# Performance work log

Hardware: AMD Instinct MI355X
Metric: run time of the kernel (lower is better)

## Reference

```python
import jax, jax.numpy as jnp
import numpy as np

B, N, C = 4, 2048, 1024
H = 16
D = C // H  # head dim = 64

def setup_inputs() -> dict:
    key = jax.random.key(0)
    k1, k2, k3 = jax.random.split(key, 3)
    x = jax.random.normal(k1, (B, N, C), dtype=jnp.float32)
    w_attn = jax.random.normal(k2, (C, 3 * C), dtype=jnp.float32) * (C ** -0.5)
    w_proj = jax.random.normal(k3, (C, C), dtype=jnp.float32) * (C ** -0.5)
    return {"x": x, "w_attn": w_attn, "w_proj": w_proj}

def reference(x, w_attn, w_proj):
    # fused QKV projection (bias=False)
    qkv = jnp.einsum('bnc,cf->bnf', x, w_attn)            # [B,N,3C]
    q, k, v = jnp.split(qkv, 3, axis=-1)                  # each [B,N,C]
    # [B,H,N,D]
    q = q.reshape(B, N, H, D).transpose(0, 2, 1, 3)
    k = k.reshape(B, N, H, D).transpose(0, 2, 1, 3)
    v = v.reshape(B, N, H, D).transpose(0, 2, 1, 3)
    # scaled dot-product attention, non-causal, no mask, dropout_p=0
    scale = 1.0 / jnp.sqrt(jnp.asarray(D, dtype=q.dtype))
    scores = jnp.einsum('bhqd,bhkd->bhqk', q, k) * scale  # [B,H,N,N]
    attn = jax.nn.softmax(scores, axis=-1)
    y = jnp.einsum('bhqk,bhkd->bhqd', attn, v)            # [B,H,N,D]
    y = y.transpose(0, 2, 1, 3).reshape(B, N, C)
    # output projection (bias=False); resid dropout is identity at p=0
    return jnp.einsum('bnc,co->bno', y, w_proj)
```

## Files before the change

kernel.cpp:

```cpp
#include <hip/hip_runtime.h>
#include <hip/hip_bf16.h>

typedef __hip_bfloat16 bf16;
typedef short short8 __attribute__((ext_vector_type(8)));
typedef float f32x4 __attribute__((ext_vector_type(4)));
typedef float f32x16 __attribute__((ext_vector_type(16)));

#define GLOBAL_AS __attribute__((address_space(1)))
#define LDS_AS __attribute__((address_space(3)))

__device__ inline unsigned short f2bf(float x) {
    union { float f; unsigned u; } v; v.f = x;
    unsigned r = v.u + 0x7fffu + ((v.u >> 16) & 1u);
    return (unsigned short)(r >> 16);
}

__device__ inline unsigned pkbf(float a, float b) {
    float2 f; f.x = a; f.y = b;
    union { __hip_bfloat162 h; unsigned u; } c;
    c.h = __float22bfloat162_rn(f);
    return c.u;
}

__device__ inline float fast_exp2(float x) {
#if __has_builtin(__builtin_amdgcn_exp2f)
    return __builtin_amdgcn_exp2f(x);
#else
    return exp2f(x);
#endif
}

__device__ inline void async16(const void* g, void* l) {
    __builtin_amdgcn_global_load_lds((const GLOBAL_AS void*)g, (LDS_AS void*)l, 16, 0, 0);
}


__global__ __launch_bounds__(256) void cvt_f32_bf16(const float* __restrict__ in,
                                                    unsigned short* __restrict__ out, int n4) {
    int i = blockIdx.x * 256 + threadIdx.x;
    if (i < n4) {
        float4 v = ((const float4*)in)[i];
        ushort4 o;
        o.x = f2bf(v.x); o.y = f2bf(v.y); o.z = f2bf(v.z); o.w = f2bf(v.w);
        ((ushort4*)out)[i] = o;
    }
}

__global__ __launch_bounds__(256) void transpose_bf16(const float* __restrict__ in,
                                                      unsigned short* __restrict__ out,
                                                      int R, int Cc) {
    __shared__ float s[32][33];
    int tx = threadIdx.x & 31, ty = threadIdx.x >> 5;
    int c0 = blockIdx.x * 32, r0 = blockIdx.y * 32;
#pragma unroll
    for (int i = 0; i < 4; i++)
        s[ty + i * 8][tx] = in[(size_t)(r0 + ty + i * 8) * Cc + c0 + tx];
    __syncthreads();
#pragma unroll
    for (int i = 0; i < 4; i++)
        out[(size_t)(c0 + ty + i * 8) * R + r0 + tx] = f2bf(s[tx][ty + i * 8]);
}


template <int MODE>
__global__ __launch_bounds__(256) void gemm_bf16(const bf16* __restrict__ A,
                                                 const bf16* __restrict__ Bt,
                                                 unsigned short* __restrict__ outQ,
                                                 unsigned short* __restrict__ outK,
                                                 unsigned short* __restrict__ outV,
                                                 float* __restrict__ outF, float qscale) {
    const int KD = 1024;
    __shared__ __align__(16) char smem[34816];
    bf16* sA = (bf16*)smem;
    bf16* sB = (bf16*)(smem + 16384);
    const int t = threadIdx.x;
    const int w = t >> 6, lane = t & 63, l15 = lane & 15, qd = lane >> 4;
    const int bn = blockIdx.x, bm = blockIdx.y;
    const int wm = (w >> 1) * 64, wn = (w & 1) * 64;
    const int sw = l15 & 7;

    f32x4 acc[4][4];
#pragma unroll
    for (int i = 0; i < 4; i++)
#pragma unroll
        for (int j = 0; j < 4; j++) acc[i][j] = (f32x4){0.f, 0.f, 0.f, 0.f};

    const int rsub = lane >> 3;
    const int csrc = ((lane & 7) ^ rsub) << 3;
    const bf16* Ab = A + (size_t)(bm * 128 + w * 32 + rsub) * KD + csrc;
    const bf16* Bb = Bt + (size_t)(bn * 128 + w * 32 + rsub) * KD + csrc;
    bf16* sAw = sA + (w * 32) * 64;
    bf16* sBw = sB + (w * 32) * 64;

    for (int kt = 0; kt < 16; ++kt) {
#pragma unroll
        for (int j = 0; j < 4; ++j) {
            async16(Ab + (size_t)(j * 8) * KD + kt * 64, sAw + j * 512);
            async16(Bb + (size_t)(j * 8) * KD + kt * 64, sBw + j * 512);
        }
        __syncthreads();
#pragma unroll
        for (int ks = 0; ks < 2; ++ks) {
            const int cphys = (((ks * 4 + qd) ^ sw) << 3);
            short8 af[4], bfv[4];
#pragma unroll
            for (int mi = 0; mi < 4; mi++)
                af[mi] = *(const short8*)&sA[(wm + mi * 16 + l15) * 64 + cphys];
#pragma unroll
            for (int ni = 0; ni < 4; ni++)
                bfv[ni] = *(const short8*)&sB[(wn + ni * 16 + l15) * 64 + cphys];
#pragma unroll
            for (int mi = 0; mi < 4; mi++)
#pragma unroll
                for (int ni = 0; ni < 4; ni++)
                    acc[mi][ni] = __builtin_amdgcn_mfma_f32_16x16x32_bf16(af[mi], bfv[ni],
                                                                          acc[mi][ni], 0, 0, 0);
        }
        __syncthreads();
    }

    if (MODE == 0) {
        unsigned short* sC = (unsigned short*)smem;
        const int part = bn >> 3;
        const int hb = (bn & 7) * 2;
        if (part < 2) {
            const float sc = (part == 0) ? qscale : 1.0f;
            unsigned short* dst = (part == 0) ? outQ : outK;
#pragma unroll
            for (int mi = 0; mi < 4; mi++)
#pragma unroll
                for (int ni = 0; ni < 4; ni++)
#pragma unroll
                    for (int r = 0; r < 4; r++)
                        sC[(wm + mi * 16 + qd * 4 + r) * 136 + wn + ni * 16 + l15] =
                            f2bf(acc[mi][ni][r] * sc);
            __syncthreads();
#pragma unroll
            for (int i = 0; i < 8; i++) {
                const int j = t + i * 256;
                const int row = j >> 4, c16 = j & 15;
                uint4 v = *(const uint4*)&sC[row * 136 + c16 * 8];
                const int m = bm * 128 + row;
                const int b = m >> 11, ns = m & 2047;
                const int h = hb + (c16 >> 3);
                const int dd = (c16 & 7) * 8;
                *(uint4*)&dst[((size_t)(b * 16 + h) * 2048 + ns) * 64 + dd] = v;
            }
        } else {
#pragma unroll
            for (int ni = 0; ni < 4; ni++)
#pragma unroll
                for (int mi = 0; mi < 4; mi++) {
                    uint2 pk;
                    pk.x = (unsigned)f2bf(acc[mi][ni][0]) | ((unsigned)f2bf(acc[mi][ni][1]) << 16);
                    pk.y = (unsigned)f2bf(acc[mi][ni][2]) | ((unsigned)f2bf(acc[mi][ni][3]) << 16);
                    *(uint2*)&sC[(wn + ni * 16 + l15) * 136 + wm + mi * 16 + qd * 4] = pk;
                }
            __syncthreads();
            const int m0b = bm * 128;
            const int b = m0b >> 11, ns0 = m0b & 2047;
#pragma unroll
            for (int i = 0; i < 8; i++) {
                const int j = t + i * 256;
                const int f = j >> 4, tc = j & 15;
                uint4 v = *(const uint4*)&sC[f * 136 + tc * 8];
                const int h = hb + (f >> 6), dd = f & 63;
                *(uint4*)&outV[((size_t)(b * 16 + h) * 64 + dd) * 2048 + ns0 + tc * 8] = v;
            }
        }
    } else {
        float* sF = (float*)smem;
#pragma unroll
        for (int pass = 0; pass < 2; ++pass) {
            if (pass) __syncthreads();
            if ((wm >> 6) == pass) {
#pragma unroll
                for (int mi = 0; mi < 4; mi++)
#pragma unroll
                    for (int ni = 0; ni < 4; ni++)
#pragma unroll
                        for (int r = 0; r < 4; r++)
                            sF[(mi * 16 + qd * 4 + r) * 132 + wn + ni * 16 + l15] =
                                acc[mi][ni][r];
            }
            __syncthreads();
#pragma unroll
            for (int i = 0; i < 8; i++) {
                const int j = t + i * 256;
                const int row = j >> 5, c4 = j & 31;
                float4 v = *(const float4*)&sF[row * 132 + c4 * 4];
                *(float4*)&outF[(size_t)(bm * 128 + pass * 64 + row) * 1024 + bn * 128 +
                                c4 * 4] = v;
            }
        }
    }
}


__global__ __launch_bounds__(512) void attn_kernel(const bf16* __restrict__ Q,
                                                   const bf16* __restrict__ K,
                                                   const bf16* __restrict__ Vt,
                                                   bf16* __restrict__ Y) {
    const int blk = blockIdx.x;
    const int bh = (blk & 7) * 8 + (blk >> 6);
    const int qt = (blk >> 3) & 7;
    const int b = bh >> 4, h16 = bh & 15;
    const int t = threadIdx.x, w = t >> 6, lane = t & 63;
    const int c = lane & 31, hl = lane >> 5;
    const int sw = c & 7;

    __shared__ __align__(16) char smem[36864];
    bf16* sK0 = (bf16*)smem;
    bf16* sK1 = (bf16*)(smem + 8192);
    bf16* sV0 = (bf16*)(smem + 16384);
    bf16* sV1 = (bf16*)(smem + 24576);
    bf16* sO = (bf16*)smem;

    const size_t bhbase = (size_t)bh * 2048 * 64;

    short8 qf[4];
#pragma unroll
    for (int kc = 0; kc < 4; kc++)
        qf[kc] = *(const short8*)(Q + bhbase + (size_t)(qt * 256 + w * 32 + c) * 64 +
                                  kc * 16 + hl * 8);

    f32x16 z16;
#pragma unroll
    for (int i = 0; i < 16; i++) z16[i] = 0.f;
    f32x16 ot[2];
#pragma unroll
    for (int i = 0; i < 16; i++) { ot[0][i] = 0.f; ot[1][i] = 0.f; }
    float l_run = 0.f;

    const int rsub = lane >> 3;
    const int cg = ((lane & 7) ^ rsub) << 3;
    const bf16* Kb = K + bhbase + (size_t)(w * 8 + rsub) * 64 + cg;
    const bf16* Vb = Vt + bhbase + (size_t)(w * 8 + rsub) * 2048 + cg;
    const int ldsoff = w * 512;

#define STAGE(ktile, sKb, sVb)                                   \
    {                                                            \
        async16(Kb + (size_t)(ktile) * 4096, (sKb) + ldsoff);    \
        async16(Vb + (size_t)(ktile) * 64,   (sVb) + ldsoff);    \
    }

    auto compute = [&](const bf16* __restrict__ sKb, const bf16* __restrict__ sVb) {
#pragma unroll
        for (int kt2 = 0; kt2 < 2; ++kt2) {
            short8 kf0 = *(const short8*)&sKb[(kt2 * 32 + c) * 64 + ((hl ^ sw) << 3)];
            __builtin_amdgcn_s_setprio(1);
            f32x16 accS = __builtin_amdgcn_mfma_f32_32x32x16_bf16(kf0, qf[0], z16, 0, 0, 0);
#pragma unroll
            for (int kc = 1; kc < 4; kc++) {
                short8 kf =
                    *(const short8*)&sKb[(kt2 * 32 + c) * 64 + (((kc * 2 + hl) ^ sw) << 3)];
                accS = __builtin_amdgcn_mfma_f32_32x32x16_bf16(kf, qf[kc], accS, 0, 0, 0);
            }
            __builtin_amdgcn_s_setprio(0);
            unsigned u[8];
            float ls = 0.f;
#pragma unroll
            for (int i = 0; i < 8; i++) {
                float p0 = fast_exp2(accS[2 * i]);
                float p1 = fast_exp2(accS[2 * i + 1]);
                ls += p0 + p1;
                u[i] = pkbf(p0, p1);
            }
            l_run += ls;
            union { uint4 u4; short8 s8; } F[2];
            F[0].u4.x = u[0]; F[0].u4.y = u[1]; F[0].u4.z = u[2]; F[0].u4.w = u[3];
            F[1].u4.x = u[4]; F[1].u4.y = u[5]; F[1].u4.z = u[6]; F[1].u4.w = u[7];
            __builtin_amdgcn_s_setprio(1);
#pragma unroll
            for (int g = 0; g < 2; ++g) {
#pragma unroll
                for (int mi2 = 0; mi2 < 2; mi2++) {
                    const bf16* vr = &sVb[(mi2 * 32 + c) * 64];
                    uint2 a0 = *(const uint2*)&vr[(((kt2 * 4 + 2 * g) ^ sw) << 3) + hl * 4];
                    uint2 a1 =
                        *(const uint2*)&vr[(((kt2 * 4 + 2 * g + 1) ^ sw) << 3) + hl * 4];
                    union { uint4 u4; short8 s8; } vf;
                    vf.u4.x = a0.x; vf.u4.y = a0.y; vf.u4.z = a1.x; vf.u4.w = a1.y;
                    ot[mi2] =
                        __builtin_amdgcn_mfma_f32_32x32x16_bf16(vf.s8, F[g].s8, ot[mi2], 0, 0, 0);
                }
            }
            __builtin_amdgcn_s_setprio(0);
        }
    };

    STAGE(0, sK0, sV0);
    for (int kt = 0; kt < 32; kt += 2) {
        __syncthreads();
        STAGE(kt + 1, sK1, sV1);
        compute(sK0, sV0);
        __syncthreads();
        if (kt + 2 < 32) STAGE(kt + 2, sK0, sV0);
        compute(sK1, sV1);
    }
    __syncthreads();

    float l = l_run + __shfl_xor(l_run, 32, 64);
    float rl = 1.f / l;
#pragma unroll
    for (int mi2 = 0; mi2 < 2; mi2++)
#pragma unroll
        for (int q4 = 0; q4 < 4; q4++) {
            const int d0 = mi2 * 32 + q4 * 8 + hl * 4;
            uint2 pk;
            pk.x = pkbf(ot[mi2][q4 * 4 + 0] * rl, ot[mi2][q4 * 4 + 1] * rl);
            pk.y = pkbf(ot[mi2][q4 * 4 + 2] * rl, ot[mi2][q4 * 4 + 3] * rl);
            *(uint2*)&sO[(w * 32 + c) * 72 + d0] = pk;
        }
    __syncthreads();
#pragma unroll
    for (int i = 0; i < 4; i++) {
        int row = (t >> 3) + i * 64, doff = (t & 7) * 8;
        uint4 vv = *(const uint4*)&sO[row * 72 + doff];
        *(uint4*)(Y + ((size_t)(b * 2048 + qt * 256 + row)) * 1024 + h16 * 64 + doff) = vv;
    }
#undef STAGE
}


extern "C" void kernel_launch(void* const* d_in, const int* in_sizes, int n_in,
                              void* d_out, int out_size, void* d_ws, size_t ws_size,
                              hipStream_t stream) {
    const float* x = (const float*)d_in[0];
    const float* w_attn = (const float*)d_in[1];
    const float* w_proj = (const float*)d_in[2];
    float* out = (float*)d_out;
    char* ws = (char*)d_ws;

    bf16* xb = (bf16*)(ws);
    bf16* waT = (bf16*)(ws + 16777216);
    bf16* wpT = (bf16*)(ws + 23068672);
    bf16* qb = (bf16*)(ws + 25165824);
    bf16* kb = (bf16*)(ws + 41943040);
    bf16* vtb = (bf16*)(ws + 58720256);

    cvt_f32_bf16<<<8192, 256, 0, stream>>>(x, (unsigned short*)xb, 2097152);
    transpose_bf16<<<dim3(96, 32), 256, 0, stream>>>(w_attn, (unsigned short*)waT, 1024, 3072);
    transpose_bf16<<<dim3(32, 32), 256, 0, stream>>>(w_proj, (unsigned short*)wpT, 1024, 1024);

    const float qscale = 0.125f * 1.44269504088896340736f;
    gemm_bf16<0><<<dim3(24, 64), 256, 0, stream>>>(xb, waT, (unsigned short*)qb,
                                                   (unsigned short*)kb, (unsigned short*)vtb,
                                                   nullptr, qscale);
    attn_kernel<<<dim3(512), 512, 0, stream>>>(qb, kb, vtb, xb );
    gemm_bf16<1><<<dim3(8, 64), 256, 0, stream>>>(xb, wpT, nullptr, nullptr, nullptr, out, 1.0f);
}
```

Baseline: 271.0 us.

## Fuse prep kernels into one launch and enlarge QKV GEMM tile to 256x128

Merges the x conversion and both weight transposes into a single launch that dispatches on block index, saving two kernel launches. The QKV projection gets its own kernel with 512 threads and a 256x128 output tile (grid halved in M), so each loaded B tile is reused across twice as many rows. The epilogue is staged in two passes through shared memory. Larger LDS use and fewer blocks (768) may lower occupancy and worsen load balance across CUs.

```diff
diff --git a/kernel.cpp b/kernel.cpp
--- a/kernel.cpp
+++ b/kernel.cpp
@@ -35,23 +35,35 @@
 }
 
 
-__global__ __launch_bounds__(256) void cvt_f32_bf16(const float* __restrict__ in,
-                                                    unsigned short* __restrict__ out, int n4) {
-    int i = blockIdx.x * 256 + threadIdx.x;
-    if (i < n4) {
-        float4 v = ((const float4*)in)[i];
+__global__ __launch_bounds__(256) void prep_fused(const float* __restrict__ x,
+                                                  unsigned short* __restrict__ xb,
+                                                  const float* __restrict__ wa,
+                                                  unsigned short* __restrict__ waT,
+                                                  const float* __restrict__ wp,
+                                                  unsigned short* __restrict__ wpT) {
+    __shared__ float s[32][33];
+    const int blk = blockIdx.x;
+    if (blk < 8192) {
+        int i = blk * 256 + threadIdx.x;
+        float4 v = ((const float4*)x)[i];
         ushort4 o;
         o.x = f2bf(v.x); o.y = f2bf(v.y); o.z = f2bf(v.z); o.w = f2bf(v.w);
-        ((ushort4*)out)[i] = o;
-    }
-}
-
-__global__ __launch_bounds__(256) void transpose_bf16(const float* __restrict__ in,
-                                                      unsigned short* __restrict__ out,
-                                                      int R, int Cc) {
-    __shared__ float s[32][33];
+        ((ushort4*)xb)[i] = o;
+        return;
+    }
+    const float* in;
+    unsigned short* out;
+    int R = 1024, Cc, c0, r0;
+    if (blk < 11264) {
+        int p = blk - 8192;
+        in = wa; out = waT; Cc = 3072;
+        c0 = (p % 96) * 32; r0 = (p / 96) * 32;
+    } else {
+        int p = blk - 11264;
+        in = wp; out = wpT; Cc = 1024;
+        c0 = (p & 31) * 32; r0 = (p >> 5) * 32;
+    }
     int tx = threadIdx.x & 31, ty = threadIdx.x >> 5;
-    int c0 = blockIdx.x * 32, r0 = blockIdx.y * 32;
 #pragma unroll
     for (int i = 0; i < 4; i++)
         s[ty + i * 8][tx] = in[(size_t)(r0 + ty + i * 8) * Cc + c0 + tx];
@@ -62,13 +74,133 @@
 }
 
 
-template <int MODE>
-__global__ __launch_bounds__(256) void gemm_bf16(const bf16* __restrict__ A,
-                                                 const bf16* __restrict__ Bt,
-                                                 unsigned short* __restrict__ outQ,
-                                                 unsigned short* __restrict__ outK,
-                                                 unsigned short* __restrict__ outV,
-                                                 float* __restrict__ outF, float qscale) {
+__global__ __launch_bounds__(512) void gemm_qkv(const bf16* __restrict__ A,
+                                                const bf16* __restrict__ Bt,
+                                                unsigned short* __restrict__ outQ,
+                                                unsigned short* __restrict__ outK,
+                                                unsigned short* __restrict__ outV,
+                                                float qscale) {
+    const int KD = 1024;
+    __shared__ __align__(16) char smem[49152];
+    bf16* sA = (bf16*)smem;
+    bf16* sB = (bf16*)(smem + 32768);
+    const int t = threadIdx.x;
+    const int w = t >> 6, lane = t & 63, l15 = lane & 15, qd = lane >> 4;
+    const int bn = blockIdx.x, bm = blockIdx.y;
+    const int wm = (w >> 1) * 64, wn = (w & 1) * 64;
+    const int sw = l15 & 7;
+
+    f32x4 acc[4][4];
+#pragma unroll
+    for (int i = 0; i < 4; i++)
+#pragma unroll
+        for (int j = 0; j < 4; j++) acc[i][j] = (f32x4){0.f, 0.f, 0.f, 0.f};
+
+    const int rsub = lane >> 3;
+    const int csrc = ((lane & 7) ^ rsub) << 3;
+    const bf16* Ab = A + (size_t)(bm * 256 + w * 32 + rsub) * KD + csrc;
+    const bf16* Bb = Bt + (size_t)(bn * 128 + w * 16 + rsub) * KD + csrc;
+    bf16* sAw = sA + (w * 32) * 64;
+    bf16* sBw = sB + (w * 16) * 64;
+
+    for (int kt = 0; kt < 16; ++kt) {
+#pragma unroll
+        for (int j = 0; j < 4; ++j)
+            async16(Ab + (size_t)(j * 8) * KD + kt * 64, sAw + j * 512);
+#pragma unroll
+        for (int j = 0; j < 2; ++j)
+            async16(Bb + (size_t)(j * 8) * KD + kt * 64, sBw + j * 512);
+        __syncthreads();
+#pragma unroll
+        for (int ks = 0; ks < 2; ++ks) {
+            const int cphys = (((ks * 4 + qd) ^ sw) << 3);
+            short8 af[4], bfv[4];
+#pragma unroll
+            for (int mi = 0; mi < 4; mi++)
+                af[mi] = *(const short8*)&sA[(wm + mi * 16 + l15) * 64 + cphys];
+#pragma unroll
+            for (int ni = 0; ni < 4; ni++)
+                bfv[ni] = *(const short8*)&sB[(wn + ni * 16 + l15) * 64 + cphys];
+#pragma unroll
+            for (int mi = 0; mi < 4; mi++)
+#pragma unroll
+                for (int ni = 0; ni < 4; ni++)
+                    acc[mi][ni] = __builtin_amdgcn_mfma_f32_16x16x32_bf16(af[mi], bfv[ni],
+                                                                          acc[mi][ni], 0, 0, 0);
+        }
+        __syncthreads();
+    }
+
+    unsigned short* sC = (unsigned short*)smem;
+    const int part = bn >> 3;
+    const int hb = (bn & 7) * 2;
+    if (part < 2) {
+        const float sc = (part == 0) ? qscale : 1.0f;
+        unsigned short* dst = (part == 0) ? outQ : outK;
+#pragma unroll
+        for (int pass = 0; pass < 2; ++pass) {
+            if (pass) __syncthreads();
+            if ((wm >> 7) == pass) {
+#pragma unroll
+                for (int mi = 0; mi < 4; mi++)
+#pragma unroll
+                    for (int ni = 0; ni < 4; ni++)
+#pragma unroll
+                        for (int r = 0; r < 4; r++)
+                            sC[((wm & 127) + mi * 16 + qd * 4 + r) * 136 + wn + ni * 16 +
+                               l15] = f2bf(acc[mi][ni][r] * sc);
+            }
+            __syncthreads();
+#pragma unroll
+            for (int i = 0; i < 4; i++) {
+                const int j = t + i * 512;
+                const int row = j >> 4, c16 = j & 15;
+                uint4 v = *(const uint4*)&sC[row * 136 + c16 * 8];
+                const int m = bm * 256 + pass * 128 + row;
+                const int b = m >> 11, ns = m & 2047;
+                const int h = hb + (c16 >> 3);
+                const int dd = (c16 & 7) * 8;
+                *(uint4*)&dst[((size_t)(b * 16 + h) * 2048 + ns) * 64 + dd] = v;
+            }
+        }
+    } else {
+        const int m0b = bm * 256;
+        const int b = m0b >> 11, ns0 = m0b & 2047;
+#pragma unroll
+        for (int pass = 0; pass < 2; ++pass) {
+            if (pass) __syncthreads();
+            if ((wm >> 7) == pass) {
+#pragma unroll
+                for (int ni = 0; ni < 4; ni++)
+#pragma unroll
+                    for (int mi = 0; mi < 4; mi++) {
+                        uint2 pk;
+                        pk.x = (unsigned)f2bf(acc[mi][ni][0]) |
+                               ((unsigned)f2bf(acc[mi][ni][1]) << 16);
+                        pk.y = (unsigned)f2bf(acc[mi][ni][2]) |
+                               ((unsigned)f2bf(acc[mi][ni][3]) << 16);
+                        *(uint2*)&sC[(wn + ni * 16 + l15) * 136 + (wm & 127) + mi * 16 +
+                                     qd * 4] = pk;
+                    }
+            }
+            __syncthreads();
+#pragma unroll
+            for (int i = 0; i < 4; i++) {
+                const int j = t + i * 512;
+                const int f = j >> 4, tc = j & 15;
+                uint4 v = *(const uint4*)&sC[f * 136 + tc * 8];
+                const int h = hb + (f >> 6), dd = f & 63;
+                *(uint4*)&outV[((size_t)(b * 16 + h) * 64 + dd) * 2048 + ns0 + pass * 128 +
+                               tc * 8] = v;
+            }
+        }
+    }
+}
+
+
+__global__ __launch_bounds__(256) void gemm_out(const bf16* __restrict__ A,
+                                                const bf16* __restrict__ Bt,
+                                                float* __restrict__ outF) {
     const int KD = 1024;
     __shared__ __align__(16) char smem[34816];
     bf16* sA = (bf16*)smem;
@@ -119,79 +251,28 @@
         __syncthreads();
     }
 
-    if (MODE == 0) {
-        unsigned short* sC = (unsigned short*)smem;
-        const int part = bn >> 3;
-        const int hb = (bn & 7) * 2;
-        if (part < 2) {
-            const float sc = (part == 0) ? qscale : 1.0f;
-            unsigned short* dst = (part == 0) ? outQ : outK;
+    float* sF = (float*)smem;
+#pragma unroll
+    for (int pass = 0; pass < 2; ++pass) {
+        if (pass) __syncthreads();
+        if ((wm >> 6) == pass) {
 #pragma unroll
             for (int mi = 0; mi < 4; mi++)
 #pragma unroll
                 for (int ni = 0; ni < 4; ni++)
 #pragma unroll
                     for (int r = 0; r < 4; r++)
-                        sC[(wm + mi * 16 + qd * 4 + r) * 136 + wn + ni * 16 + l15] =
-                            f2bf(acc[mi][ni][r] * sc);
-            __syncthreads();
-#pragma unroll
-            for (int i = 0; i < 8; i++) {
-                const int j = t + i * 256;
-                const int row = j >> 4, c16 = j & 15;
-                uint4 v = *(const uint4*)&sC[row * 136 + c16 * 8];
-                const int m = bm * 128 + row;
-                const int b = m >> 11, ns = m & 2047;
-                const int h = hb + (c16 >> 3);
-                const int dd = (c16 & 7) * 8;
-                *(uint4*)&dst[((size_t)(b * 16 + h) * 2048 + ns) * 64 + dd] = v;
-            }
-        } else {
-#pragma unroll
-            for (int ni = 0; ni < 4; ni++)
-#pragma unroll
-                for (int mi = 0; mi < 4; mi++) {
-                    uint2 pk;
-                    pk.x = (unsigned)f2bf(acc[mi][ni][0]) | ((unsigned)f2bf(acc[mi][ni][1]) << 16);
-                    pk.y = (unsigned)f2bf(acc[mi][ni][2]) | ((unsigned)f2bf(acc[mi][ni][3]) << 16);
-                    *(uint2*)&sC[(wn + ni * 16 + l15) * 136 + wm + mi * 16 + qd * 4] = pk;
-                }
-            __syncthreads();
-            const int m0b = bm * 128;
-            const int b = m0b >> 11, ns0 = m0b & 2047;
-#pragma unroll
-            for (int i = 0; i < 8; i++) {
-                const int j = t + i * 256;
-                const int f = j >> 4, tc = j & 15;
-                uint4 v = *(const uint4*)&sC[f * 136 + tc * 8];
-                const int h = hb + (f >> 6), dd = f & 63;
-                *(uint4*)&outV[((size_t)(b * 16 + h) * 64 + dd) * 2048 + ns0 + tc * 8] = v;
-            }
-        }
-    } else {
-        float* sF = (float*)smem;
-#pragma unroll
-        for (int pass = 0; pass < 2; ++pass) {
-            if (pass) __syncthreads();
-            if ((wm >> 6) == pass) {
-#pragma unroll
-                for (int mi = 0; mi < 4; mi++)
-#pragma unroll
-                    for (int ni = 0; ni < 4; ni++)
-#pragma unroll
-                        for (int r = 0; r < 4; r++)
-                            sF[(mi * 16 + qd * 4 + r) * 132 + wn + ni * 16 + l15] =
-                                acc[mi][ni][r];
-            }
-            __syncthreads();
-#pragma unroll
-            for (int i = 0; i < 8; i++) {
-                const int j = t + i * 256;
-                const int row = j >> 5, c4 = j & 31;
-                float4 v = *(const float4*)&sF[row * 132 + c4 * 4];
-                *(float4*)&outF[(size_t)(bm * 128 + pass * 64 + row) * 1024 + bn * 128 +
-                                c4 * 4] = v;
-            }
+                        sF[(mi * 16 + qd * 4 + r) * 132 + wn + ni * 16 + l15] =
+                            acc[mi][ni][r];
+        }
+        __syncthreads();
+#pragma unroll
+        for (int i = 0; i < 8; i++) {
+            const int j = t + i * 256;
+            const int row = j >> 5, c4 = j & 31;
+            float4 v = *(const float4*)&sF[row * 132 + c4 * 4];
+            *(float4*)&outF[(size_t)(bm * 128 + pass * 64 + row) * 1024 + bn * 128 + c4 * 4] =
+                v;
         }
     }
 }
@@ -339,14 +420,14 @@
     bf16* kb = (bf16*)(ws + 41943040);
     bf16* vtb = (bf16*)(ws + 58720256);
 
-    cvt_f32_bf16<<<8192, 256, 0, stream>>>(x, (unsigned short*)xb, 2097152);
-    transpose_bf16<<<dim3(96, 32), 256, 0, stream>>>(w_attn, (unsigned short*)waT, 1024, 3072);
-    transpose_bf16<<<dim3(32, 32), 256, 0, stream>>>(w_proj, (unsigned short*)wpT, 1024, 1024);
+    prep_fused<<<12288, 256, 0, stream>>>(x, (unsigned short*)xb, w_attn,
+                                          (unsigned short*)waT, w_proj,
+                                          (unsigned short*)wpT);
 
     const float qscale = 0.125f * 1.44269504088896340736f;
-    gemm_bf16<0><<<dim3(24, 64), 256, 0, stream>>>(xb, waT, (unsigned short*)qb,
-                                                   (unsigned short*)kb, (unsigned short*)vtb,
-                                                   nullptr, qscale);
+    gemm_qkv<<<dim3(24, 32), 512, 0, stream>>>(xb, waT, (unsigned short*)qb,
+                                               (unsigned short*)kb, (unsigned short*)vtb,
+                                               qscale);
     attn_kernel<<<dim3(512), 512, 0, stream>>>(qb, kb, vtb, xb );
-    gemm_bf16<1><<<dim3(8, 64), 256, 0, stream>>>(xb, wpT, nullptr, nullptr, nullptr, out, 1.0f);
-}
+    gemm_out<<<dim3(8, 64), 256, 0, stream>>>(xb, wpT, out);
+}
```

New measurement: 274.5 us. No clear change (+1.3%).
